# Kernel tuning notes

Measured on AMD Instinct MI355X. Metric: run time of the kernel, lower is better.

The kernel has to match this reference:

```python
import jax, jax.numpy as jnp
import numpy as np

IMG = 840.0
MIN_SIZES = [[16.0, 32.0], [64.0, 128.0], [256.0, 512.0]]
STEPS = [8, 16, 32]
THRESH = 0.35      # neg_overlap / matching threshold used by this repo's MultiBoxLoss
NEG_POS = 7
LOC_WEIGHT = 2.0
VAR0, VAR1 = 0.1, 0.2


def _make_priors():
    out = []
    for ms, step in zip(MIN_SIZES, STEPS):
        f = int(np.ceil(IMG / step))
        jj, ii = np.meshgrid(np.arange(f), np.arange(f))  # j: cols (x), i: rows (y)
        cx = (jj + 0.5) * step / IMG
        cy = (ii + 0.5) * step / IMG
        for m in ms:
            s = np.full_like(cx, m / IMG)
            out.append(np.stack([cx, cy, s, s], axis=-1).reshape(-1, 4))
    return np.concatenate(out, axis=0).astype(np.float32)  # [29126, 4] (cx, cy, w, h)


def setup_inputs() -> dict:
    key = jax.random.key(0)
    k1, k2, k3, k4 = jax.random.split(key, 4)
    B, G = 64, 24
    priors = jnp.asarray(_make_priors())            # [P, 4]
    P = priors.shape[0]
    loc_data = 0.1 * jax.random.normal(k1, (B, P, 4), dtype=jnp.float32)
    conf_data = jax.random.normal(k2, (B, P, 2), dtype=jnp.float32)
    cxy = jax.random.uniform(k3, (B, G, 2), minval=0.2, maxval=0.8)
    wh = jax.random.uniform(k4, (B, G, 2), minval=0.05, maxval=0.3)
    gt_boxes = jnp.clip(jnp.concatenate([cxy - wh / 2, cxy + wh / 2], axis=-1), 1e-3, 1.0)
    gt_labels = jnp.ones((B, G), dtype=jnp.int32)   # single foreground class (num_classes=2)
    return {"loc_data": loc_data, "conf_data": conf_data, "gt_boxes": gt_boxes,
            "gt_labels": gt_labels, "priors": priors}


def _multibox_loss(loc_data, conf_data, gt_boxes, gt_labels, priors):
    B, P, _ = loc_data.shape
    G = gt_boxes.shape[1]
    # priors in point form for IoU
    pr_pt = jnp.concatenate([priors[:, :2] - priors[:, 2:] / 2,
                             priors[:, :2] + priors[:, 2:] / 2], axis=1)  # [P,4]
    area_p = (pr_pt[:, 2] - pr_pt[:, 0]) * (pr_pt[:, 3] - pr_pt[:, 1])

    def match_one(truths, labels):
        # IoU [G, P]
        lt = jnp.maximum(truths[:, None, :2], pr_pt[None, :, :2])
        rb = jnp.minimum(truths[:, None, 2:], pr_pt[None, :, 2:])
        wh = jnp.clip(rb - lt, 0.0)
        inter = wh[..., 0] * wh[..., 1]
        area_t = (truths[:, 2] - truths[:, 0]) * (truths[:, 3] - truths[:, 1])
        iou = inter / (area_t[:, None] + area_p[None, :] - inter)
        best_prior_idx = jnp.argmax(iou, axis=1)          # [G]
        bto = jnp.max(iou, axis=0)                        # [P] best truth overlap
        bti = jnp.argmax(iou, axis=0)                     # [P] best truth idx
        bto = bto.at[best_prior_idx].set(2.0)             # ensure each gt keeps its best prior
        bti = bti.at[best_prior_idx].set(jnp.arange(G))
        matched = truths[bti]                             # [P,4]
        conf = jnp.where(bto < THRESH, 0, labels[bti])    # [P]
        # encode (SSD style, variances 0.1/0.2)
        g_cxcy = ((matched[:, :2] + matched[:, 2:]) / 2 - priors[:, :2]) / (VAR0 * priors[:, 2:])
        g_wh = jnp.log((matched[:, 2:] - matched[:, :2]) / priors[:, 2:]) / VAR1
        return jnp.concatenate([g_cxcy, g_wh], axis=1), conf

    loc_t, conf_t = jax.vmap(match_one)(gt_boxes, gt_labels)  # [B,P,4], [B,P]
    pos = conf_t > 0                                          # [B,P]

    # localization: smooth L1 over positives
    diff = jnp.abs(loc_data - loc_t)
    sl1 = jnp.where(diff < 1.0, 0.5 * diff * diff, diff - 0.5)
    loss_l = jnp.sum(sl1 * pos[..., None].astype(loc_data.dtype))

    # per-prior CE = logsumexp - logit[target]
    lse = jax.nn.logsumexp(conf_data, axis=-1)                               # [B,P]
    gold = jnp.take_along_axis(conf_data, conf_t[..., None], axis=-1)[..., 0]
    ce_all = lse - gold                                                      # [B,P]

    # hard negative mining: rank background-class loss of negatives
    mine = jnp.where(pos, 0.0, ce_all)
    rank = jnp.argsort(jnp.argsort(-mine, axis=1), axis=1)
    num_pos = jnp.sum(pos, axis=1, keepdims=True)                            # [B,1]
    num_neg = jnp.minimum(NEG_POS * num_pos, P - 1)
    neg = rank < num_neg

    mask = pos | neg
    loss_c = jnp.sum(jnp.where(mask, ce_all, 0.0))

    N = jnp.maximum(jnp.sum(pos).astype(loc_data.dtype), 1.0)
    return loss_l / N, loss_c / N


def reference(loc_data, conf_data, gt_boxes, gt_labels, priors):
    loss_l, loss_c = _multibox_loss(loc_data, conf_data, gt_boxes, gt_labels, priors)
    return LOC_WEIGHT * loss_l + loss_c
```

## Files before the change

kernel.cpp:

```cpp
#include <hip/hip_runtime.h>

static constexpr int B_ = 64;
static constexpr int P_ = 29126;
static constexpr int G_ = 24;
static constexpr float THRESH_ = 0.35f;
static constexpr int NEGPOS_ = 7;
static constexpr int PBL_ = (P_ + 1023) / 1024;
static constexpr int NBL_ = PBL_ * B_;
static constexpr int WPB_ = 912;
static constexpr int CCS_ = 32;

__device__ const float LAD_[16] = {
    -0.5f, -0.2f, 0.0f, 0.2f, 0.4f, 0.6f, 0.8f, 1.0f,
     1.2f,  1.4f, 1.6f, 1.8f, 2.1f, 2.4f, 2.8f, 3.3f };

static constexpr size_t ZBYTES_ =
    (size_t)B_*WPB_*4*2 + (size_t)B_*CCS_*4 + 16;
static constexpr int ZVEC_ = (int)((ZBYTES_ + 15) / 16);

__device__ inline unsigned zmap(float z) {
    const unsigned f = __float_as_uint(z);
    return (f & 0x80000000u) ? ~f : (f | 0x80000000u);
}
__device__ inline float zunmap(unsigned u) {
    const unsigned f = (u & 0x80000000u) ? (u & 0x7FFFFFFFu) : ~u;
    return __uint_as_float(f);
}

__global__ __launch_bounds__(256) void k_zero(ulonglong2* __restrict__ dst)
{
    const int i = blockIdx.x*256 + threadIdx.x;
    if (i < ZVEC_) dst[i] = make_ulonglong2(0ull, 0ull);
}

__global__ __launch_bounds__(256) void k_sparse(
    const float4* __restrict__ gt4,
    const float4* __restrict__ priors4,
    unsigned* __restrict__ matchw,
    unsigned long long* __restrict__ bp_pack)
{
    const int g = blockIdx.x;
    const int b = blockIdx.y;
    const int bg = b*G_ + g;
    const int tid = threadIdx.x;

    const float4 t = gt4[bg];
    const float area_t = (t.z - t.x) * (t.w - t.y);

    float bv = -1.0f; int bq = 0;

#pragma unroll
    for (int r = 0; r < 6; ++r) {
        const int   f    = (r < 2) ? 105 : (r < 4) ? 53 : 27;
        const float sc   = (r < 2) ? 105.0f : (r < 4) ? 52.5f : 26.25f;
        const int   base = (r == 0) ? 0 : (r == 1) ? 11025 : (r == 2) ? 22050
                         : (r == 3) ? 24859 : (r == 4) ? 27668 : 28397;
        const float hw   = ((r == 0) ? 16.0f : (r == 1) ? 32.0f : (r == 2) ? 64.0f
                         : (r == 3) ? 128.0f : (r == 4) ? 256.0f : 512.0f)
                           * (0.5f / 840.0f);

        const int j0 = max(0,     (int)floorf((t.x - hw)*sc - 0.5f) - 1);
        const int j1 = min(f - 1, (int)ceilf ((t.z + hw)*sc - 0.5f) + 1);
        const int i0 = max(0,     (int)floorf((t.y - hw)*sc - 0.5f) - 1);
        const int i1 = min(f - 1, (int)ceilf ((t.w + hw)*sc - 0.5f) + 1);
        const int W = j1 - j0 + 1;
        const int n = W * (i1 - i0 + 1);

        for (int c = tid; c < n; c += 256) {
            const int ii = c / W;
            const int jj = c - ii*W;
            const int p = base + (i0 + ii)*f + (j0 + jj);
            const float4 pr = priors4[p];
            const float hx = pr.z * 0.5f, hy = pr.w * 0.5f;
            const float px0 = pr.x - hx, py0 = pr.y - hy;
            const float px1 = pr.x + hx, py1 = pr.y + hy;
            const float area_p = (px1 - px0) * (py1 - py0);
            const float lx = fmaxf(t.x, px0), ly = fmaxf(t.y, py0);
            const float rx = fminf(t.z, px1), ry = fminf(t.w, py1);
            const float iw = fmaxf(rx - lx, 0.0f), ih = fmaxf(ry - ly, 0.0f);
            const float inter = iw * ih;
            const float iou = __fdividef(inter, (area_t + area_p) - inter);

            if (iou >= THRESH_)
                atomicOr(&matchw[b*WPB_ + (p >> 5)], 1u << (p & 31));
            if (iou > bv) { bv = iou; bq = p; }
        }
    }

    const int lane = tid & 63, wave = tid >> 6;
    for (int m = 32; m; m >>= 1) {
        const float ov = __shfl_xor(bv, m, 64);
        const int   oq = __shfl_xor(bq, m, 64);
        if (ov > bv || (ov == bv && oq < bq)) { bv = ov; bq = oq; }
    }
    __shared__ float swv[4];
    __shared__ int   swq[4];
    if (lane == 0) { swv[wave] = bv; swq[wave] = bq; }
    __syncthreads();
    if (tid == 0) {
        float v = swv[0]; int q = swq[0];
#pragma unroll
        for (int w = 1; w < 4; ++w)
            if (swv[w] > v || (swv[w] == v && swq[w] < q)) { v = swv[w]; q = swq[w]; }
        bp_pack[bg] = (v >= 0.0f)
            ? (((unsigned long long)__float_as_uint(v) << 32)
               | (unsigned long long)(~(unsigned int)q))
            : 0ull;
    }
}

__global__ __launch_bounds__(256) void k_count(
    const float4* __restrict__ loc4,
    const float2* __restrict__ conf2,
    const float4* __restrict__ gt4,
    const int* __restrict__ labels,
    const float4* __restrict__ priors4,
    const unsigned* __restrict__ matchw,
    unsigned* __restrict__ posw,
    const unsigned long long* __restrict__ bp_pack,
    float* __restrict__ pl, float* __restrict__ pc, int* __restrict__ pp,
    unsigned int* __restrict__ pcnt)
{
    const int b = blockIdx.y;
    const int tid = threadIdx.x;
    const int lane = tid & 63, wave = tid >> 6;
    const int pbase = blockIdx.x*1024;

    __shared__ float4 sgt[G_];
    __shared__ float  sarea[G_];
    __shared__ int    slab[G_];
    __shared__ int    sovr[1024];
    if (tid < G_) {
        const float4 t = gt4[b*G_ + tid];
        sgt[tid] = t;
        sarea[tid] = (t.z - t.x) * (t.w - t.y);
        slab[tid] = labels[b*G_ + tid];
    }
    for (int i = tid; i < 1024; i += 256) sovr[i] = -1;
    __syncthreads();
    if (tid < G_) {
        const unsigned long long pk = bp_pack[b*G_ + tid];
        const int q = (int)(~(unsigned int)(pk & 0xFFFFFFFFull)) - pbase;
        if (q >= 0 && q < 1024) atomicMax(&sovr[q], tid);
    }
    __syncthreads();

    const int p0 = pbase + tid*4;
    float lL = 0.0f, pce = 0.0f; int np = 0;
    unsigned q0 = 0, q1 = 0, q2 = 0, q3 = 0, q4 = 0, q5 = 0, q6 = 0, q7 = 0;

    if (p0 < P_) {
        const unsigned mw = (matchw[b*WPB_ + (p0 >> 5)] >> (p0 & 31)) & 0xFu;
        const int4 ov4 = *(const int4*)&sovr[tid*4];
        const int og[4] = { ov4.x, ov4.y, ov4.z, ov4.w };
        const bool full = (p0 + 3 < P_);

        float cf[8];
        if (full) {
            const float4* c4 = (const float4*)conf2;
            const size_t base2 = ((size_t)b*P_ + p0) >> 1;
            const float4 ca = c4[base2];
            const float4 cb = c4[base2 + 1];
            cf[0]=ca.x; cf[1]=ca.y; cf[2]=ca.z; cf[3]=ca.w;
            cf[4]=cb.x; cf[5]=cb.y; cf[6]=cb.z; cf[7]=cb.w;
        } else {
            for (int c = 0; c < 4; ++c) {
                if (p0 + c < P_) {
                    const float2 x = conf2[(size_t)b*P_ + p0 + c];
                    cf[2*c] = x.x; cf[2*c+1] = x.y;
                } else { cf[2*c] = -1e30f; cf[2*c+1] = -1e30f; }
            }
        }

        float z4[4];
#pragma unroll
        for (int c = 0; c < 4; ++c)
            z4[c] = (p0 + c < P_) ? (cf[2*c+1] - cf[2*c])
                                  : -__int_as_float(0x7F800000);

        unsigned spec = 0;
#pragma unroll
        for (int c = 0; c < 4; ++c)
            if (og[c] >= 0 || ((mw >> c) & 1u)) spec |= (1u << c);

        if (__any(spec != 0u)) {
            unsigned posbits = 0;
#pragma unroll
            for (int c = 0; c < 4; ++c) {
                const int p = p0 + c;
                if (((spec >> c) & 1u) && p < P_) {
                    int cc = 0, g = 0;
                    if (og[c] >= 0) { g = og[c]; cc = slab[g]; }
                    else {
                        const float4 pr = priors4[p];
                        const float hx = pr.z * 0.5f, hy = pr.w * 0.5f;
                        const float px0 = pr.x - hx, py0 = pr.y - hy;
                        const float px1 = pr.x + hx, py1 = pr.y + hy;
                        const float area_p = (px1 - px0) * (py1 - py0);
                        float best = -1.0f;
#pragma unroll
                        for (int gg = 0; gg < G_; ++gg) {
                            const float4 t = sgt[gg];
                            const float lx = fmaxf(t.x, px0), ly = fmaxf(t.y, py0);
                            const float rx = fminf(t.z, px1), ry = fminf(t.w, py1);
                            const float iw = fmaxf(rx - lx, 0.0f), ih = fmaxf(ry - ly, 0.0f);
                            const float inter = iw * ih;
                            const float iou = __fdividef(inter, (sarea[gg] + area_p) - inter);
                            if (iou > best) { best = iou; g = gg; }
                        }
                        cc = slab[g];
                    }
                    if (cc > 0) {
                        const float ce = __logf(1.0f + __expf(cf[2*c] - cf[2*c+1]));
                        np += 1; pce += ce;
                        z4[c] = -__int_as_float(0x7F800000);
                        posbits |= (1u << (p0 & 31)) << c;
                        const float4 t  = sgt[g];
                        const float4 pr = priors4[p];
                        const float gcx = __fdividef((t.x + t.z)*0.5f - pr.x, 0.1f*pr.z);
                        const float gcy = __fdividef((t.y + t.w)*0.5f - pr.y, 0.1f*pr.w);
                        const float gw  = __logf(__fdividef(t.z - t.x, pr.z)) * 5.0f;
                        const float gh  = __logf(__fdividef(t.w - t.y, pr.w)) * 5.0f;
                        const float4 l = loc4[(size_t)b*P_ + p];
                        const float d0 = fabsf(l.x - gcx);
                        const float d1 = fabsf(l.y - gcy);
                        const float d2 = fabsf(l.z - gw);
                        const float d3 = fabsf(l.w - gh);
                        lL += (d0 < 1.0f) ? 0.5f*d0*d0 : d0 - 0.5f;
                        lL += (d1 < 1.0f) ? 0.5f*d1*d1 : d1 - 0.5f;
                        lL += (d2 < 1.0f) ? 0.5f*d2*d2 : d2 - 0.5f;
                        lL += (d3 < 1.0f) ? 0.5f*d3*d3 : d3 - 0.5f;
                    }
                }
            }
            if (posbits) atomicOr(&posw[b*WPB_ + (p0 >> 5)], posbits);
        }

#pragma unroll
        for (int c = 0; c < 4; ++c) {
            const float z = z4[c];
            q0 += (unsigned)(z > -0.5f) + ((unsigned)(z > -0.2f) << 16);
            q1 += (unsigned)(z >  0.0f) + ((unsigned)(z >  0.2f) << 16);
            q2 += (unsigned)(z >  0.4f) + ((unsigned)(z >  0.6f) << 16);
            q3 += (unsigned)(z >  0.8f) + ((unsigned)(z >  1.0f) << 16);
            q4 += (unsigned)(z >  1.2f) + ((unsigned)(z >  1.4f) << 16);
            q5 += (unsigned)(z >  1.6f) + ((unsigned)(z >  1.8f) << 16);
            q6 += (unsigned)(z >  2.1f) + ((unsigned)(z >  2.4f) << 16);
            q7 += (unsigned)(z >  2.8f) + ((unsigned)(z >  3.3f) << 16);
        }
    }

    for (int m = 32; m; m >>= 1) {
        lL  += __shfl_xor(lL, m, 64);
        pce += __shfl_xor(pce, m, 64);
        np  += __shfl_xor(np, m, 64);
        q0 += __shfl_xor(q0, m, 64); q1 += __shfl_xor(q1, m, 64);
        q2 += __shfl_xor(q2, m, 64); q3 += __shfl_xor(q3, m, 64);
        q4 += __shfl_xor(q4, m, 64); q5 += __shfl_xor(q5, m, 64);
        q6 += __shfl_xor(q6, m, 64); q7 += __shfl_xor(q7, m, 64);
    }
    __shared__ float swL[4], swC[4];
    __shared__ int   swP[4];
    __shared__ unsigned swu[4][8];
    if (lane == 0) {
        swL[wave] = lL; swC[wave] = pce; swP[wave] = np;
        swu[wave][0] = q0; swu[wave][1] = q1; swu[wave][2] = q2; swu[wave][3] = q3;
        swu[wave][4] = q4; swu[wave][5] = q5; swu[wave][6] = q6; swu[wave][7] = q7;
    }
    __syncthreads();
    const int o = b*PBL_ + blockIdx.x;
    if (tid == 0) {
        pl[o] = swL[0] + swL[1] + swL[2] + swL[3];
        pc[o] = swC[0] + swC[1] + swC[2] + swC[3];
        pp[o] = swP[0] + swP[1] + swP[2] + swP[3];
    }
    if (tid < 8)
        pcnt[o*8 + tid] = swu[0][tid] + swu[1][tid] + swu[2][tid] + swu[3][tid];
}

__device__ inline void bracket_block(
    const unsigned int* __restrict__ pcnt, const int* __restrict__ pp,
    int b, int tid, int4* out, int* np_out)
{
    __shared__ int sred[256];
    sred[tid] = (tid < PBL_) ? pp[b*PBL_ + tid] : 0;
    __syncthreads();
    for (int off = 128; off > 0; off >>= 1) {
        if (tid < off) sred[tid] += sred[tid+off];
        __syncthreads();
    }
    const int np = sred[0];
    int k = NEGPOS_ * np; if (k > P_-1) k = P_-1;

    __shared__ unsigned red[32][8];
    {
        const int i = tid >> 3, j = tid & 7;
        red[i][j] = (i < PBL_) ? pcnt[(b*PBL_ + i)*8 + j] : 0u;
    }
    __syncthreads();
    for (int off = 16; off > 0; off >>= 1) {
        const int i = tid >> 3, j = tid & 7;
        if (i < off) red[i][j] += red[i+off][j];
        __syncthreads();
    }
    __shared__ int C[16];
    if (tid < 8) {
        C[2*tid]   = (int)(red[0][tid] & 0xFFFFu);
        C[2*tid+1] = (int)(red[0][tid] >> 16);
    }
    __shared__ int4 sbr;
    __syncthreads();
    if (tid == 0) {
        int4 s; s.w = 0;
        if (k <= 0) {
            s.x = 0x7F800000; s.y = 0x7F800000; s.z = 0;
        } else {
            int js = -1;
            for (int j = 0; j < 16; ++j) if (C[j] >= k) js = j;
            if (js < 0) {
                s.x = __float_as_int(LAD_[0]);
                s.y = (int)0xFF800000;
                s.z = k - C[0];
            } else if (js == 15) {
                s.x = 0x7F800000;
                s.y = __float_as_int(LAD_[15]);
                s.z = k;
            } else {
                s.x = __float_as_int(LAD_[js+1]);
                s.y = __float_as_int(LAD_[js]);
                s.z = k - C[js+1];
            }
        }
        sbr = s;
    }
    __syncthreads();
    *out = sbr;
    *np_out = np;
}

__global__ __launch_bounds__(256) void k_collect(
    const float2* __restrict__ conf2,
    const unsigned* __restrict__ posw,
    const unsigned int* __restrict__ pcnt, const int* __restrict__ pp,
    unsigned int* __restrict__ cand, int* __restrict__ candCount,
    float* __restrict__ pcol)
{
    const int b = blockIdx.y;
    const int tid = threadIdx.x;
    const int lane = tid & 63;

    int4 se; int np_dummy;
    bracket_block(pcnt, pp, b, tid, &se, &np_dummy);
    const float hi = __int_as_float(se.x);
    const float lo = __int_as_float(se.y);

    __shared__ unsigned int sbuf[1024];
    __shared__ int scnt;
    __shared__ int gbase;
    if (tid == 0) scnt = 0;
    __syncthreads();

    const int p0 = blockIdx.x*1024 + tid*4;
    float z4[4] = { -__int_as_float(0x7F800000), -__int_as_float(0x7F800000),
                    -__int_as_float(0x7F800000), -__int_as_float(0x7F800000) };
    if (p0 < P_) {
        const unsigned pw = (posw[b*WPB_ + (p0 >> 5)] >> (p0 & 31)) & 0xFu;
        if (p0 + 3 < P_) {
            const float4* c4 = (const float4*)conf2;
            const size_t base2 = ((size_t)b*P_ + p0) >> 1;
            const float4 ca = c4[base2];
            const float4 cb = c4[base2 + 1];
            z4[0] = ca.y - ca.x; z4[1] = ca.w - ca.z;
            z4[2] = cb.y - cb.x; z4[3] = cb.w - cb.z;
        } else {
            for (int c = 0; c < 4; ++c) {
                if (p0 + c < P_) {
                    const float2 x = conf2[(size_t)b*P_ + p0 + c];
                    z4[c] = x.y - x.x;
                }
            }
        }
#pragma unroll
        for (int c = 0; c < 4; ++c)
            if ((pw >> c) & 1u) z4[c] = -__int_as_float(0x7F800000);
    }

    float sum = 0.0f;
#pragma unroll
    for (int c = 0; c < 4; ++c) {
        const float z = z4[c];
        bool isCand = false;
        if (z > hi) sum += __logf(1.0f + __expf(z));
        else isCand = (z > lo);
        const unsigned long long mask = __ballot(isCand);
        const int wcnt = __popcll(mask);
        int wbase = 0;
        if (lane == 0 && wcnt) wbase = atomicAdd(&scnt, wcnt);
        wbase = __shfl(wbase, 0, 64);
        if (isCand) {
            const int before = __popcll(mask & ((1ull << lane) - 1ull));
            sbuf[wbase + before] = zmap(z);
        }
    }
    __syncthreads();
    const int tot = scnt;
    if (tid == 0) gbase = tot ? atomicAdd(&candCount[b*CCS_], tot) : 0;
    __syncthreads();
    for (int i = tid; i < tot; i += 256)
        cand[(size_t)b*P_ + gbase + i] = sbuf[i];

    __shared__ float sf2[256];
    sf2[tid] = sum;
    __syncthreads();
    for (int off = 128; off > 0; off >>= 1) {
        if (tid < off) sf2[tid] += sf2[tid+off];
        __syncthreads();
    }
    if (tid == 0) pcol[b*PBL_ + blockIdx.x] = sf2[0];
}

__global__ __launch_bounds__(256) void k_sel2fin(
    const unsigned int* __restrict__ cand, const int* __restrict__ candCount,
    const unsigned int* __restrict__ pcnt, const int* __restrict__ pp,
    const float* __restrict__ pl, const float* __restrict__ pc,
    const float* __restrict__ pcol,
    float4* __restrict__ outb, unsigned int* __restrict__ ticket,
    float* __restrict__ out)
{
    const int b = blockIdx.x;
    const int tid = threadIdx.x;

    int4 se; int np;
    bracket_block(pcnt, pp, b, tid, &se, &np);
    const int kk = se.z;

    __shared__ float rA[256], rB[256], rC2[256];
    rA[tid]  = (tid < PBL_) ? pl[b*PBL_ + tid] : 0.0f;
    rB[tid]  = (tid < PBL_) ? pc[b*PBL_ + tid] : 0.0f;
    rC2[tid] = (tid < PBL_) ? pcol[b*PBL_ + tid] : 0.0f;
    __syncthreads();
    for (int off = 128; off > 0; off >>= 1) {
        if (tid < off) {
            rA[tid] += rA[tid+off];
            rB[tid] += rB[tid+off];
            rC2[tid] += rC2[tid+off];
        }
        __syncthreads();
    }
    const float sumL = rA[0], sumC = rB[0], sumhi = rC2[0];
    __syncthreads();

    float ctopv = sumhi;
    const int nc = candCount[b*CCS_];
    if (kk > 0 && nc > 0) {
        const unsigned int* row = cand + (size_t)b * P_;
        __shared__ unsigned int hist[256];
        __shared__ unsigned int sc0[256], sc1[256];
        __shared__ unsigned int sh_prefix;
        __shared__ int sh_kk;

        unsigned int prefix = 0; int kk2 = kk;
        for (int pass = 3; pass >= 0; --pass) {
            hist[tid] = 0;
            __syncthreads();
            const unsigned int highmask =
                (pass == 3) ? 0u : (0xFFFFFFFFu << ((pass+1)*8));
            for (int i = tid; i < nc; i += 256) {
                const unsigned int u = row[i];
                if ((u & highmask) == (prefix & highmask))
                    atomicAdd(&hist[(u >> (pass*8)) & 255u], 1u);
            }
            __syncthreads();
            sc0[tid] = hist[255 - tid];
            __syncthreads();
            unsigned int* src = sc0; unsigned int* dst = sc1;
            for (int off = 1; off < 256; off <<= 1) {
                unsigned int v = src[tid];
                if (tid >= off) v += src[tid - off];
                dst[tid] = v;
                __syncthreads();
                unsigned int* t2 = src; src = dst; dst = t2;
            }
            {
                const int bin = 255 - tid;
                const int cum = (int)src[tid];
                const int cumPrev = (tid == 0) ? 0 : (int)src[tid-1];
                if (cum >= kk2 && cumPrev < kk2) {
                    sh_prefix = prefix | ((unsigned int)bin << (pass*8));
                    sh_kk = kk2 - cumPrev;
                }
            }
            __syncthreads();
            prefix = sh_prefix; kk2 = sh_kk;
            __syncthreads();
        }

        const float zT = zunmap(prefix);
        const float T = __logf(1.0f + __expf(zT));
        float sum = 0.0f; int cnt = 0;
        for (int i = tid; i < nc; i += 256) {
            const unsigned int u = row[i];
            if (u > prefix) {
                sum += __logf(1.0f + __expf(zunmap(u)));
                ++cnt;
            }
        }
        __shared__ float sf[256];
        __shared__ int   sci[256];
        sf[tid] = sum; sci[tid] = cnt;
        __syncthreads();
        for (int off = 128; off > 0; off >>= 1) {
            if (tid < off) { sf[tid] += sf[tid+off]; sci[tid] += sci[tid+off]; }
            __syncthreads();
        }
        ctopv = sumhi + sf[0] + (float)(kk - sci[0]) * T;
    }

    __shared__ int sdone;
    if (tid == 0) {
        outb[b] = make_float4(sumL, sumC, (float)np, ctopv);
        __threadfence();
        sdone = (int)atomicAdd(ticket, 1u);
    }
    __syncthreads();
    if (sdone == B_ - 1) {
        __threadfence();
        float L = 0.0f, C = 0.0f, Pn = 0.0f, T = 0.0f;
        if (tid < B_) {
            const float4 v = outb[tid];
            L = v.x; C = v.y; Pn = v.z; T = v.w;
        }
        for (int m = 32; m; m >>= 1) {
            L += __shfl_xor(L, m, 64);
            C += __shfl_xor(C, m, 64);
            Pn += __shfl_xor(Pn, m, 64);
            T += __shfl_xor(T, m, 64);
        }
        if (tid == 0)
            out[0] = (2.0f*L + C + T) / fmaxf(Pn, 1.0f);
    }
}

extern "C" void kernel_launch(void* const* d_in, const int* in_sizes, int n_in,
                              void* d_out, int out_size, void* d_ws, size_t ws_size,
                              hipStream_t stream)
{
    const float* loc    = (const float*)d_in[0];
    const float* conf   = (const float*)d_in[1];
    const float* gt     = (const float*)d_in[2];
    const int*   labels = (const int*)d_in[3];
    const float* priors = (const float*)d_in[4];
    float* out = (float*)d_out;

    char* ws = (char*)d_ws;
    size_t off = 0;
    unsigned* matchw = (unsigned*)(ws + off);        off += (size_t)B_*WPB_*4;
    unsigned* posw   = (unsigned*)(ws + off);        off += (size_t)B_*WPB_*4;
    int* candCount = (int*)(ws + off);               off += (size_t)B_*CCS_*4;
    unsigned int* ticket = (unsigned int*)(ws + off); off += 16;
    off = (off + 255) & ~255ull;
    unsigned long long* bp_pack =
        (unsigned long long*)(ws + off);             off += (size_t)B_*G_*8;
    float* pl   = (float*)(ws + off);                off += (size_t)NBL_*4;
    float* pc   = (float*)(ws + off);                off += (size_t)NBL_*4;
    int*   pp   = (int*)(ws + off);                  off += (size_t)NBL_*4;
    float* pcol = (float*)(ws + off);                off += (size_t)NBL_*4;
    unsigned int* pcnt = (unsigned int*)(ws + off);  off += (size_t)NBL_*8*4;
    unsigned int* cand = (unsigned int*)(ws + off);  off += (size_t)B_*P_*4;
    float4* outb = (float4*)(ws + off);              off += (size_t)B_*16;

    k_zero<<<dim3((ZVEC_ + 255)/256), dim3(256), 0, stream>>>((ulonglong2*)ws);
    k_sparse<<<dim3(G_, B_), dim3(256), 0, stream>>>(
        (const float4*)gt, (const float4*)priors, matchw, bp_pack);
    k_count<<<dim3(PBL_, B_), dim3(256), 0, stream>>>(
        (const float4*)loc, (const float2*)conf, (const float4*)gt, labels,
        (const float4*)priors, matchw, posw, bp_pack, pl, pc, pp, pcnt);
    k_collect<<<dim3(PBL_, B_), dim3(256), 0, stream>>>(
        (const float2*)conf, posw, pcnt, pp, cand, candCount, pcol);
    k_sel2fin<<<dim3(B_), dim3(256), 0, stream>>>(
        cand, candCount, pcnt, pp, pl, pc, pcol, outb, ticket, out);
}
```

Before: 73.14 us.

## Fuse collect and final selection via per-batch tickets; double chunk size per block

Each block now covers 2048 priors (8 per thread) instead of 1024, giving 15 chunks per batch row. The collect kernel and the selection/finalize kernel are merged: the last collect block of each batch, found through a per-batch atomic ticket, runs the selection and the final reduction. This removes one kernel launch and a redundant bracket computation. In exchange the grid has fewer blocks with more work each, and the tail of each batch row is serialized behind the ticket.

```diff
diff --git a/kernel.cpp b/kernel.cpp
--- a/kernel.cpp
+++ b/kernel.cpp
@@ -5,8 +5,8 @@
 static constexpr int G_ = 24;
 static constexpr float THRESH_ = 0.35f;
 static constexpr int NEGPOS_ = 7;
-static constexpr int PBL_ = (P_ + 1023) / 1024;
-static constexpr int NBL_ = PBL_ * B_;
+static constexpr int NCH_ = 15;
+static constexpr int NBL_ = NCH_ * B_;
 static constexpr int WPB_ = 912;
 static constexpr int CCS_ = 32;
 
@@ -15,7 +15,7 @@
      1.2f,  1.4f, 1.6f, 1.8f, 2.1f, 2.4f, 2.8f, 3.3f };
 
 static constexpr size_t ZBYTES_ =
-    (size_t)B_*WPB_*4*2 + (size_t)B_*CCS_*4 + 16;
+    (size_t)B_*WPB_*4*2 + (size_t)B_*CCS_*4*2 + 16;
 static constexpr int ZVEC_ = (int)((ZBYTES_ + 15) / 16);
 
 __device__ inline unsigned zmap(float z) {
@@ -124,69 +124,75 @@
     const int b = blockIdx.y;
     const int tid = threadIdx.x;
     const int lane = tid & 63, wave = tid >> 6;
-    const int pbase = blockIdx.x*1024;
+    const int pbase = blockIdx.x*2048;
 
     __shared__ float4 sgt[G_];
     __shared__ float  sarea[G_];
     __shared__ int    slab[G_];
-    __shared__ int    sovr[1024];
+    __shared__ int    sovr[2048];
     if (tid < G_) {
         const float4 t = gt4[b*G_ + tid];
         sgt[tid] = t;
         sarea[tid] = (t.z - t.x) * (t.w - t.y);
         slab[tid] = labels[b*G_ + tid];
     }
-    for (int i = tid; i < 1024; i += 256) sovr[i] = -1;
+    for (int i = tid; i < 2048; i += 256) sovr[i] = -1;
     __syncthreads();
     if (tid < G_) {
         const unsigned long long pk = bp_pack[b*G_ + tid];
         const int q = (int)(~(unsigned int)(pk & 0xFFFFFFFFull)) - pbase;
-        if (q >= 0 && q < 1024) atomicMax(&sovr[q], tid);
-    }
-    __syncthreads();
-
-    const int p0 = pbase + tid*4;
+        if (q >= 0 && q < 2048) atomicMax(&sovr[q], tid);
+    }
+    __syncthreads();
+
+    const int p0 = pbase + tid*8;
     float lL = 0.0f, pce = 0.0f; int np = 0;
     unsigned q0 = 0, q1 = 0, q2 = 0, q3 = 0, q4 = 0, q5 = 0, q6 = 0, q7 = 0;
 
     if (p0 < P_) {
-        const unsigned mw = (matchw[b*WPB_ + (p0 >> 5)] >> (p0 & 31)) & 0xFu;
-        const int4 ov4 = *(const int4*)&sovr[tid*4];
-        const int og[4] = { ov4.x, ov4.y, ov4.z, ov4.w };
-        const bool full = (p0 + 3 < P_);
-
-        float cf[8];
+        const unsigned mw = (matchw[b*WPB_ + (p0 >> 5)] >> (p0 & 31)) & 0xFFu;
+        const int4 ovA = *(const int4*)&sovr[tid*8];
+        const int4 ovB = *(const int4*)&sovr[tid*8 + 4];
+        const int og[8] = { ovA.x, ovA.y, ovA.z, ovA.w,
+                            ovB.x, ovB.y, ovB.z, ovB.w };
+        const bool full = (p0 + 7 < P_);
+
+        float cf[16];
         if (full) {
             const float4* c4 = (const float4*)conf2;
             const size_t base2 = ((size_t)b*P_ + p0) >> 1;
             const float4 ca = c4[base2];
             const float4 cb = c4[base2 + 1];
-            cf[0]=ca.x; cf[1]=ca.y; cf[2]=ca.z; cf[3]=ca.w;
-            cf[4]=cb.x; cf[5]=cb.y; cf[6]=cb.z; cf[7]=cb.w;
+            const float4 cc2 = c4[base2 + 2];
+            const float4 cd = c4[base2 + 3];
+            cf[0]=ca.x;  cf[1]=ca.y;  cf[2]=ca.z;  cf[3]=ca.w;
+            cf[4]=cb.x;  cf[5]=cb.y;  cf[6]=cb.z;  cf[7]=cb.w;
+            cf[8]=cc2.x; cf[9]=cc2.y; cf[10]=cc2.z; cf[11]=cc2.w;
+            cf[12]=cd.x; cf[13]=cd.y; cf[14]=cd.z;  cf[15]=cd.w;
         } else {
-            for (int c = 0; c < 4; ++c) {
+            for (int c = 0; c < 8; ++c) {
                 if (p0 + c < P_) {
                     const float2 x = conf2[(size_t)b*P_ + p0 + c];
                     cf[2*c] = x.x; cf[2*c+1] = x.y;
-                } else { cf[2*c] = -1e30f; cf[2*c+1] = -1e30f; }
-            }
-        }
-
-        float z4[4];
-#pragma unroll
-        for (int c = 0; c < 4; ++c)
-            z4[c] = (p0 + c < P_) ? (cf[2*c+1] - cf[2*c])
+                } else { cf[2*c] = 0.0f; cf[2*c+1] = 0.0f; }
+            }
+        }
+
+        float z8[8];
+#pragma unroll
+        for (int c = 0; c < 8; ++c)
+            z8[c] = (p0 + c < P_) ? (cf[2*c+1] - cf[2*c])
                                   : -__int_as_float(0x7F800000);
 
         unsigned spec = 0;
 #pragma unroll
-        for (int c = 0; c < 4; ++c)
+        for (int c = 0; c < 8; ++c)
             if (og[c] >= 0 || ((mw >> c) & 1u)) spec |= (1u << c);
 
         if (__any(spec != 0u)) {
             unsigned posbits = 0;
 #pragma unroll
-            for (int c = 0; c < 4; ++c) {
+            for (int c = 0; c < 8; ++c) {
                 const int p = p0 + c;
                 if (((spec >> c) & 1u) && p < P_) {
                     int cc = 0, g = 0;
@@ -213,8 +219,8 @@
                     if (cc > 0) {
                         const float ce = __logf(1.0f + __expf(cf[2*c] - cf[2*c+1]));
                         np += 1; pce += ce;
-                        z4[c] = -__int_as_float(0x7F800000);
-                        posbits |= (1u << (p0 & 31)) << c;
+                        z8[c] = -__int_as_float(0x7F800000);
+                        posbits |= 1u << ((p0 & 31) + c);
                         const float4 t  = sgt[g];
                         const float4 pr = priors4[p];
                         const float gcx = __fdividef((t.x + t.z)*0.5f - pr.x, 0.1f*pr.z);
@@ -237,8 +243,8 @@
         }
 
 #pragma unroll
-        for (int c = 0; c < 4; ++c) {
-            const float z = z4[c];
+        for (int c = 0; c < 8; ++c) {
+            const float z = z8[c];
             q0 += (unsigned)(z > -0.5f) + ((unsigned)(z > -0.2f) << 16);
             q1 += (unsigned)(z >  0.0f) + ((unsigned)(z >  0.2f) << 16);
             q2 += (unsigned)(z >  0.4f) + ((unsigned)(z >  0.6f) << 16);
@@ -268,7 +274,7 @@
         swu[wave][4] = q4; swu[wave][5] = q5; swu[wave][6] = q6; swu[wave][7] = q7;
     }
     __syncthreads();
-    const int o = b*PBL_ + blockIdx.x;
+    const int o = b*NCH_ + blockIdx.x;
     if (tid == 0) {
         pl[o] = swL[0] + swL[1] + swL[2] + swL[3];
         pc[o] = swC[0] + swC[1] + swC[2] + swC[3];
@@ -283,7 +289,7 @@
     int b, int tid, int4* out, int* np_out)
 {
     __shared__ int sred[256];
-    sred[tid] = (tid < PBL_) ? pp[b*PBL_ + tid] : 0;
+    sred[tid] = (tid < NCH_) ? pp[b*NCH_ + tid] : 0;
     __syncthreads();
     for (int off = 128; off > 0; off >>= 1) {
         if (tid < off) sred[tid] += sred[tid+off];
@@ -295,7 +301,7 @@
     __shared__ unsigned red[32][8];
     {
         const int i = tid >> 3, j = tid & 7;
-        red[i][j] = (i < PBL_) ? pcnt[(b*PBL_ + i)*8 + j] : 0u;
+        red[i][j] = (i < NCH_) ? pcnt[(b*NCH_ + i)*8 + j] : 0u;
     }
     __syncthreads();
     for (int off = 16; off > 0; off >>= 1) {
@@ -338,57 +344,66 @@
     *np_out = np;
 }
 
-__global__ __launch_bounds__(256) void k_collect(
+__global__ __launch_bounds__(256) void k_colfin(
     const float2* __restrict__ conf2,
     const unsigned* __restrict__ posw,
     const unsigned int* __restrict__ pcnt, const int* __restrict__ pp,
+    const float* __restrict__ pl, const float* __restrict__ pc,
+    float* __restrict__ pcol,
     unsigned int* __restrict__ cand, int* __restrict__ candCount,
-    float* __restrict__ pcol)
+    int* __restrict__ ticketB, unsigned int* __restrict__ ticketG,
+    float4* __restrict__ outb, float* __restrict__ out)
 {
     const int b = blockIdx.y;
     const int tid = threadIdx.x;
     const int lane = tid & 63;
 
-    int4 se; int np_dummy;
-    bracket_block(pcnt, pp, b, tid, &se, &np_dummy);
+    int4 se; int np;
+    bracket_block(pcnt, pp, b, tid, &se, &np);
     const float hi = __int_as_float(se.x);
     const float lo = __int_as_float(se.y);
-
-    __shared__ unsigned int sbuf[1024];
+    const int kk = se.z;
+
+    __shared__ unsigned int sbuf[2048];
     __shared__ int scnt;
     __shared__ int gbase;
     if (tid == 0) scnt = 0;
     __syncthreads();
 
-    const int p0 = blockIdx.x*1024 + tid*4;
-    float z4[4] = { -__int_as_float(0x7F800000), -__int_as_float(0x7F800000),
-                    -__int_as_float(0x7F800000), -__int_as_float(0x7F800000) };
+    const int p0 = blockIdx.x*2048 + tid*8;
+    float z8[8];
+#pragma unroll
+    for (int c = 0; c < 8; ++c) z8[c] = -__int_as_float(0x7F800000);
     if (p0 < P_) {
-        const unsigned pw = (posw[b*WPB_ + (p0 >> 5)] >> (p0 & 31)) & 0xFu;
-        if (p0 + 3 < P_) {
+        const unsigned pw = (posw[b*WPB_ + (p0 >> 5)] >> (p0 & 31)) & 0xFFu;
+        if (p0 + 7 < P_) {
             const float4* c4 = (const float4*)conf2;
             const size_t base2 = ((size_t)b*P_ + p0) >> 1;
             const float4 ca = c4[base2];
             const float4 cb = c4[base2 + 1];
-            z4[0] = ca.y - ca.x; z4[1] = ca.w - ca.z;
-            z4[2] = cb.y - cb.x; z4[3] = cb.w - cb.z;
+            const float4 cc2 = c4[base2 + 2];
+            const float4 cd = c4[base2 + 3];
+            z8[0] = ca.y - ca.x;  z8[1] = ca.w - ca.z;
+            z8[2] = cb.y - cb.x;  z8[3] = cb.w - cb.z;
+            z8[4] = cc2.y - cc2.x; z8[5] = cc2.w - cc2.z;
+            z8[6] = cd.y - cd.x;  z8[7] = cd.w - cd.z;
         } else {
-            for (int c = 0; c < 4; ++c) {
+            for (int c = 0; c < 8; ++c) {
                 if (p0 + c < P_) {
                     const float2 x = conf2[(size_t)b*P_ + p0 + c];
-                    z4[c] = x.y - x.x;
+                    z8[c] = x.y - x.x;
                 }
             }
         }
 #pragma unroll
-        for (int c = 0; c < 4; ++c)
-            if ((pw >> c) & 1u) z4[c] = -__int_as_float(0x7F800000);
+        for (int c = 0; c < 8; ++c)
+            if ((pw >> c) & 1u) z8[c] = -__int_as_float(0x7F800000);
     }
 
     float sum = 0.0f;
 #pragma unroll
-    for (int c = 0; c < 4; ++c) {
-        const float z = z4[c];
+    for (int c = 0; c < 8; ++c) {
+        const float z = z8[c];
         bool isCand = false;
         if (z > hi) sum += __logf(1.0f + __expf(z));
         else isCand = (z > lo);
@@ -416,28 +431,21 @@
         if (tid < off) sf2[tid] += sf2[tid+off];
         __syncthreads();
     }
-    if (tid == 0) pcol[b*PBL_ + blockIdx.x] = sf2[0];
-}
-
-__global__ __launch_bounds__(256) void k_sel2fin(
-    const unsigned int* __restrict__ cand, const int* __restrict__ candCount,
-    const unsigned int* __restrict__ pcnt, const int* __restrict__ pp,
-    const float* __restrict__ pl, const float* __restrict__ pc,
-    const float* __restrict__ pcol,
-    float4* __restrict__ outb, unsigned int* __restrict__ ticket,
-    float* __restrict__ out)
-{
-    const int b = blockIdx.x;
-    const int tid = threadIdx.x;
-
-    int4 se; int np;
-    bracket_block(pcnt, pp, b, tid, &se, &np);
-    const int kk = se.z;
+    if (tid == 0) pcol[b*NCH_ + blockIdx.x] = sf2[0];
+
+    __shared__ int sdoneB;
+    if (tid == 0) {
+        __threadfence();
+        sdoneB = atomicAdd(&ticketB[b*CCS_], 1);
+    }
+    __syncthreads();
+    if (sdoneB != NCH_ - 1) return;
+    __threadfence();
 
     __shared__ float rA[256], rB[256], rC2[256];
-    rA[tid]  = (tid < PBL_) ? pl[b*PBL_ + tid] : 0.0f;
-    rB[tid]  = (tid < PBL_) ? pc[b*PBL_ + tid] : 0.0f;
-    rC2[tid] = (tid < PBL_) ? pcol[b*PBL_ + tid] : 0.0f;
+    rA[tid]  = (tid < NCH_) ? pl[b*NCH_ + tid] : 0.0f;
+    rB[tid]  = (tid < NCH_) ? pc[b*NCH_ + tid] : 0.0f;
+    rC2[tid] = (tid < NCH_) ? pcol[b*NCH_ + tid] : 0.0f;
     __syncthreads();
     for (int off = 128; off > 0; off >>= 1) {
         if (tid < off) {
@@ -497,17 +505,17 @@
 
         const float zT = zunmap(prefix);
         const float T = __logf(1.0f + __expf(zT));
-        float sum = 0.0f; int cnt = 0;
+        float s2 = 0.0f; int cnt = 0;
         for (int i = tid; i < nc; i += 256) {
             const unsigned int u = row[i];
             if (u > prefix) {
-                sum += __logf(1.0f + __expf(zunmap(u)));
+                s2 += __logf(1.0f + __expf(zunmap(u)));
                 ++cnt;
             }
         }
         __shared__ float sf[256];
         __shared__ int   sci[256];
-        sf[tid] = sum; sci[tid] = cnt;
+        sf[tid] = s2; sci[tid] = cnt;
         __syncthreads();
         for (int off = 128; off > 0; off >>= 1) {
             if (tid < off) { sf[tid] += sf[tid+off]; sci[tid] += sci[tid+off]; }
@@ -516,14 +524,14 @@
         ctopv = sumhi + sf[0] + (float)(kk - sci[0]) * T;
     }
 
-    __shared__ int sdone;
+    __shared__ int sdoneG;
     if (tid == 0) {
         outb[b] = make_float4(sumL, sumC, (float)np, ctopv);
         __threadfence();
-        sdone = (int)atomicAdd(ticket, 1u);
-    }
-    __syncthreads();
-    if (sdone == B_ - 1) {
+        sdoneG = (int)atomicAdd(ticketG, 1u);
+    }
+    __syncthreads();
+    if (sdoneG == B_ - 1) {
         __threadfence();
         float L = 0.0f, C = 0.0f, Pn = 0.0f, T = 0.0f;
         if (tid < B_) {
@@ -557,7 +565,8 @@
     unsigned* matchw = (unsigned*)(ws + off);        off += (size_t)B_*WPB_*4;
     unsigned* posw   = (unsigned*)(ws + off);        off += (size_t)B_*WPB_*4;
     int* candCount = (int*)(ws + off);               off += (size_t)B_*CCS_*4;
-    unsigned int* ticket = (unsigned int*)(ws + off); off += 16;
+    int* ticketB   = (int*)(ws + off);               off += (size_t)B_*CCS_*4;
+    unsigned int* ticketG = (unsigned int*)(ws + off); off += 16;
     off = (off + 255) & ~255ull;
     unsigned long long* bp_pack =
         (unsigned long long*)(ws + off);             off += (size_t)B_*G_*8;
@@ -572,11 +581,10 @@
     k_zero<<<dim3((ZVEC_ + 255)/256), dim3(256), 0, stream>>>((ulonglong2*)ws);
     k_sparse<<<dim3(G_, B_), dim3(256), 0, stream>>>(
         (const float4*)gt, (const float4*)priors, matchw, bp_pack);
-    k_count<<<dim3(PBL_, B_), dim3(256), 0, stream>>>(
+    k_count<<<dim3(NCH_, B_), dim3(256), 0, stream>>>(
         (const float4*)loc, (const float2*)conf, (const float4*)gt, labels,
         (const float4*)priors, matchw, posw, bp_pack, pl, pc, pp, pcnt);
-    k_collect<<<dim3(PBL_, B_), dim3(256), 0, stream>>>(
-        (const float2*)conf, posw, pcnt, pp, cand, candCount, pcol);
-    k_sel2fin<<<dim3(B_), dim3(256), 0, stream>>>(
-        cand, candCount, pcnt, pp, pl, pc, pcol, outb, ticket, out);
-}
+    k_colfin<<<dim3(NCH_, B_), dim3(256), 0, stream>>>(
+        (const float2*)conf, posw, pcnt, pp, pl, pc, pcol,
+        cand, candCount, ticketB, ticketG, outb, out);
+}
```

Result: slower. 113.0 us (+54.5%).
